# Performance work log

Measured on AMD Instinct MI355X. Metric: run time of the kernel, lower is better.

## Reference

```python
import jax, jax.numpy as jnp
import numpy as np

N = 32768      # input points
P = 16         # num_points (kernel points == max neighbors per center)
NC = 8192      # centers after fps(ratio=0.25)
E = NC * P     # edges (exactly P neighbors per center, grouped by center)
IN_F = 64
OUT_F = 128
RADIUS = 1.0
KP_EXTENT = RADIUS / 1.5


def setup_inputs() -> dict:
    key = jax.random.key(0)
    k1, k2, k3, k4, k5 = jax.random.split(key, 5)
    x = jax.random.normal(k1, (N, IN_F), dtype=jnp.float32)
    pos = jax.random.normal(k2, (N, 3), dtype=jnp.float32)
    edge_src = jax.random.randint(k3, (E,), 0, N, dtype=jnp.int32)
    # edges grouped contiguously per center, P edges each (radius() output layout)
    edge_tgt = (jnp.arange(E, dtype=jnp.int32) // P)
    # kernel point positions inside the ball of radius KP-layout scale
    kernel_pts = jax.random.uniform(k4, (P, 3), dtype=jnp.float32,
                                    minval=-0.66 * RADIUS, maxval=0.66 * RADIUS)
    # kaiming-uniform-like init for [P, in, out] per-kernel-point weights
    bound = 1.0 / np.sqrt(IN_F)
    kernel_weight = jax.random.uniform(k5, (P, IN_F, OUT_F), dtype=jnp.float32,
                                       minval=-bound, maxval=bound)
    return {"x": x, "pos": pos, "edge_src": edge_src, "edge_tgt": edge_tgt,
            "kernel_pts": kernel_pts, "kernel_weight": kernel_weight}


def reference(x, pos, edge_src, edge_tgt, kernel_pts, kernel_weight):
    n_edges = edge_src.shape[0]
    nc = n_edges // P
    # gather endpoints (message_x_and_pos: pos_i, pos_j, x_j)
    pos_i = pos[edge_tgt]                       # [E,3]
    pos_j = pos[edge_src]                       # [E,3]
    rel = (pos_i - pos_j).reshape(nc, P, 3)     # neighbors, [NC,P,3]
    # distances from every neighbor to every kernel point
    diff = rel[:, :, None, :] - kernel_pts[None, None, :, :]   # [NC,P,K,3]
    sq = jnp.sum(diff * diff, axis=-1)                          # [NC,P,K]
    # linear KP influence, clamped at 0
    all_w = jnp.maximum(1.0 - jnp.sqrt(sq) / KP_EXTENT, 0.0)
    # one-hot argmin kernel assignment (VQ-like selection)
    nn_idx = jnp.argmin(sq, axis=-1)                            # [NC,P]
    one_hot = jax.nn.one_hot(nn_idx, P, dtype=all_w.dtype)      # [NC,P,K]
    all_w = all_w * one_hot
    feat = x[edge_src].reshape(nc, P, IN_F)                     # [NC,P,in]
    # weighted_features = all_w @ feat  (contract kernel axis vs neighbor axis)
    wf = jnp.einsum('cnk,cki->cni', all_w, feat)                # [NC,P,in]
    # per-edge matmul with the argmin-selected weight matrix; one_hot selects
    # W[nn_idx] without materializing the [E,in,out] gather
    msg = jnp.einsum('cni,cnk,kio->cno', wf, one_hot, kernel_weight)  # [NC,P,out]
    # scatter-add aggregation over target centers (MessagePassing aggr='add')
    out = jax.ops.segment_sum(msg.reshape(-1, OUT_F), edge_tgt, num_segments=NC)
    return out
```

## Files before the change

kernel.cpp:

```cpp
#include <hip/hip_runtime.h>
#include <hip/hip_bf16.h>


#define P 16
#define IN_F 64
#define OUT_F 128
#define NCC 8192
#define KPE 0.6666667f

typedef short short8 __attribute__((ext_vector_type(8)));
typedef float floatx4 __attribute__((ext_vector_type(4)));

__device__ inline unsigned short f2bf(float f) {
    __hip_bfloat16 h = __float2bfloat16(f);
    return __builtin_bit_cast(unsigned short, h);
}

__global__ __launch_bounds__(256) void kconv_w(const float* __restrict__ Wf,
                                               unsigned short* __restrict__ Wb) {
    __shared__ float T[64][129];
    const int m = blockIdx.x;
    const int t = threadIdx.x;
#pragma unroll
    for (int it = 0; it < 32; ++it) {
        const int idx = it * 256 + t;
        T[idx >> 7][idx & 127] = Wf[m * 8192 + idx];
    }
    __syncthreads();
#pragma unroll
    for (int it = 0; it < 32; ++it) {
        const int idx = it * 256 + t;
        Wb[m * 8192 + idx] = f2bf(T[idx & 63][idx >> 6]);
    }
}

__global__ __launch_bounds__(256, 2) void kconv_main(
    const float* __restrict__ x, const float* __restrict__ pos,
    const int* __restrict__ esrc, const int* __restrict__ etgt,
    const float* __restrict__ kpts, const unsigned short* __restrict__ Wb,
    float* __restrict__ out)
{
    __shared__ float kps[48];
    __shared__ float wv[256];
    __shared__ int   nnv[256];
    __shared__ float sT[256];
    __shared__ int   srcT[256];
    __shared__ __align__(16) unsigned short A_lds[16 * 1024];

    const int t  = threadIdx.x;
    const int c0 = blockIdx.x * 16;

    if (t < 48) kps[t] = kpts[t];

    const int e   = c0 * P + t;
    const int src = esrc[e];
    const int tgt = etgt[e];
    float rx = __fsub_rn(pos[tgt * 3 + 0], pos[src * 3 + 0]);
    float ry = __fsub_rn(pos[tgt * 3 + 1], pos[src * 3 + 1]);
    float rz = __fsub_rn(pos[tgt * 3 + 2], pos[src * 3 + 2]);
    __syncthreads();
    float best = 1e30f; int nn = 0;
#pragma unroll
    for (int k = 0; k < 16; ++k) {
        float dx = __fsub_rn(rx, kps[k * 3 + 0]);
        float dy = __fsub_rn(ry, kps[k * 3 + 1]);
        float dz = __fsub_rn(rz, kps[k * 3 + 2]);
        float sq = __fadd_rn(__fadd_rn(__fmul_rn(dx, dx), __fmul_rn(dy, dy)),
                             __fmul_rn(dz, dz));
        if (sq < best) { best = sq; nn = k; }
    }
    float w = fmaxf(__fsub_rn(1.0f, __fdiv_rn(__fsqrt_rn(best), KPE)), 0.0f);
    wv[t] = w; nnv[t] = nn;
    srcT[(t & 15) * 16 + (t >> 4)] = src;
    __syncthreads();

    {
        const int cl = t >> 4, mm = t & 15;
        float sacc = 0.f;
#pragma unroll
        for (int n2 = 0; n2 < 16; ++n2) {
            const int idx = cl * 16 + n2;
            sacc += (nnv[idx] == mm) ? wv[idx] : 0.f;
        }
        sT[mm * 16 + cl] = sacc;
    }
    __syncthreads();

    const float4* x4 = reinterpret_cast<const float4*>(x);
    {
        const int row  = t & 15;
        const int m    = t >> 4;
        const int srow = srcT[m * 16 + row];
        const float sv = sT[m * 16 + row];
        const int xb   = srow * 16;
        char* Ab = reinterpret_cast<char*>(A_lds);
        const int rbase = row * 2048;
        const int swz   = (row & 7) << 4;
#pragma unroll
        for (int p = 0; p < 4; ++p) {
            const float4 v0 = x4[xb + p * 4 + 0];
            const float4 v1 = x4[xb + p * 4 + 1];
            const float4 v2 = x4[xb + p * 4 + 2];
            const float4 v3 = x4[xb + p * 4 + 3];
            short8 pk0, pk1;
            pk0[0] = (short)f2bf(sv * v0.x); pk0[1] = (short)f2bf(sv * v0.y);
            pk0[2] = (short)f2bf(sv * v0.z); pk0[3] = (short)f2bf(sv * v0.w);
            pk0[4] = (short)f2bf(sv * v1.x); pk0[5] = (short)f2bf(sv * v1.y);
            pk0[6] = (short)f2bf(sv * v1.z); pk0[7] = (short)f2bf(sv * v1.w);
            pk1[0] = (short)f2bf(sv * v2.x); pk1[1] = (short)f2bf(sv * v2.y);
            pk1[2] = (short)f2bf(sv * v2.z); pk1[3] = (short)f2bf(sv * v2.w);
            pk1[4] = (short)f2bf(sv * v3.x); pk1[5] = (short)f2bf(sv * v3.y);
            pk1[6] = (short)f2bf(sv * v3.z); pk1[7] = (short)f2bf(sv * v3.w);
            const int kb = m * 128 + p * 32;
            *reinterpret_cast<short8*>(Ab + rbase + ((kb)      ^ swz)) = pk0;
            *reinterpret_cast<short8*>(Ab + rbase + ((kb + 16) ^ swz)) = pk1;
        }
    }
    __syncthreads();

    const short8* wb8 = reinterpret_cast<const short8*>(Wb);
    const char*   Ab  = reinterpret_cast<const char*>(A_lds);

    const int lane = t & 63;
    const int cgi  = t >> 6;
    const int quad = lane >> 4, l16 = lane & 15;

    const int arow = l16 * 2048;
    const int aswz = (l16 & 7) << 4;
    const int bc0  = cgi * 32 + l16;
    const int bc1  = bc0 + 16;

    floatx4 acc0 = {0.f, 0.f, 0.f, 0.f};
    floatx4 acc1 = {0.f, 0.f, 0.f, 0.f};

#pragma unroll
    for (int m = 0; m < 16; ++m) {
        const short8 a0 = *reinterpret_cast<const short8*>(
            Ab + arow + ((m * 128 + quad * 16) ^ aswz));
        const short8 a1 = *reinterpret_cast<const short8*>(
            Ab + arow + ((m * 128 + 64 + quad * 16) ^ aswz));
        const short8 b00 = wb8[(m * 128 + bc0) * 8 + quad];
        const short8 b01 = wb8[(m * 128 + bc0) * 8 + quad + 4];
        const short8 b10 = wb8[(m * 128 + bc1) * 8 + quad];
        const short8 b11 = wb8[(m * 128 + bc1) * 8 + quad + 4];
        acc0 = __builtin_amdgcn_mfma_f32_16x16x32_bf16(a0, b00, acc0, 0, 0, 0);
        acc1 = __builtin_amdgcn_mfma_f32_16x16x32_bf16(a0, b10, acc1, 0, 0, 0);
        acc0 = __builtin_amdgcn_mfma_f32_16x16x32_bf16(a1, b01, acc0, 0, 0, 0);
        acc1 = __builtin_amdgcn_mfma_f32_16x16x32_bf16(a1, b11, acc1, 0, 0, 0);
    }

    const int colbase = cgi * 32 + l16;
    const int rowbase = c0 + quad * 4;
#pragma unroll
    for (int v = 0; v < 4; ++v) {
        out[(rowbase + v) * 128 + colbase]      = acc0[v];
        out[(rowbase + v) * 128 + colbase + 16] = acc1[v];
    }
}

extern "C" void kernel_launch(void* const* d_in, const int* in_sizes, int n_in,
                              void* d_out, int out_size, void* d_ws, size_t ws_size,
                              hipStream_t stream) {
    const float* x    = (const float*)d_in[0];
    const float* pos  = (const float*)d_in[1];
    const int*   esrc = (const int*)d_in[2];
    const int*   etgt = (const int*)d_in[3];
    const float* kpts = (const float*)d_in[4];
    const float* Wf   = (const float*)d_in[5];
    float* out = (float*)d_out;
    unsigned short* Wb = (unsigned short*)d_ws;

    hipLaunchKernelGGL(kconv_w, dim3(16), dim3(256), 0, stream, Wf, Wb);
    hipLaunchKernelGGL(kconv_main, dim3(NCC / 16), dim3(256), 0, stream,
                       x, pos, esrc, etgt, kpts, Wb, out);
}
```

Before: 91.93 us.

## Parallelize weight conversion and coalesce feature gather into A tile

The weight bf16 transpose kernel now runs on 512 blocks with one element per thread instead of 16 blocks staging through shared memory. This trades uncoalesced strided reads for far more parallelism on a tiny kernel. The feature gather is reorganized so 16 consecutive threads each load one float4 of the same source row, giving coalesced 256-byte row reads instead of each thread streaming a full row. The MFMA loop is changed from full unroll to unroll 4, which may reduce register pressure.

```diff
diff --git a/kernel.cpp b/kernel.cpp
--- a/kernel.cpp
+++ b/kernel.cpp
@@ -18,20 +18,11 @@
 
 __global__ __launch_bounds__(256) void kconv_w(const float* __restrict__ Wf,
                                                unsigned short* __restrict__ Wb) {
-    __shared__ float T[64][129];
-    const int m = blockIdx.x;
-    const int t = threadIdx.x;
-#pragma unroll
-    for (int it = 0; it < 32; ++it) {
-        const int idx = it * 256 + t;
-        T[idx >> 7][idx & 127] = Wf[m * 8192 + idx];
-    }
-    __syncthreads();
-#pragma unroll
-    for (int it = 0; it < 32; ++it) {
-        const int idx = it * 256 + t;
-        Wb[m * 8192 + idx] = f2bf(T[idx & 63][idx >> 6]);
-    }
+    int tg = blockIdx.x * 256 + threadIdx.x;
+    int m = tg >> 13;
+    int n = (tg >> 6) & 127;
+    int i = tg & 63;
+    Wb[tg] = f2bf(Wf[(m * 64 + i) * 128 + n]);
 }
 
 __global__ __launch_bounds__(256, 2) void kconv_main(
@@ -88,32 +79,19 @@
 
     const float4* x4 = reinterpret_cast<const float4*>(x);
     {
-        const int row  = t & 15;
-        const int m    = t >> 4;
-        const int srow = srcT[m * 16 + row];
-        const float sv = sT[m * 16 + row];
-        const int xb   = srow * 16;
+        const int row = t >> 4, aq = t & 15;
         char* Ab = reinterpret_cast<char*>(A_lds);
         const int rbase = row * 2048;
         const int swz   = (row & 7) << 4;
 #pragma unroll
-        for (int p = 0; p < 4; ++p) {
-            const float4 v0 = x4[xb + p * 4 + 0];
-            const float4 v1 = x4[xb + p * 4 + 1];
-            const float4 v2 = x4[xb + p * 4 + 2];
-            const float4 v3 = x4[xb + p * 4 + 3];
-            short8 pk0, pk1;
-            pk0[0] = (short)f2bf(sv * v0.x); pk0[1] = (short)f2bf(sv * v0.y);
-            pk0[2] = (short)f2bf(sv * v0.z); pk0[3] = (short)f2bf(sv * v0.w);
-            pk0[4] = (short)f2bf(sv * v1.x); pk0[5] = (short)f2bf(sv * v1.y);
-            pk0[6] = (short)f2bf(sv * v1.z); pk0[7] = (short)f2bf(sv * v1.w);
-            pk1[0] = (short)f2bf(sv * v2.x); pk1[1] = (short)f2bf(sv * v2.y);
-            pk1[2] = (short)f2bf(sv * v2.z); pk1[3] = (short)f2bf(sv * v2.w);
-            pk1[4] = (short)f2bf(sv * v3.x); pk1[5] = (short)f2bf(sv * v3.y);
-            pk1[6] = (short)f2bf(sv * v3.z); pk1[7] = (short)f2bf(sv * v3.w);
-            const int kb = m * 128 + p * 32;
-            *reinterpret_cast<short8*>(Ab + rbase + ((kb)      ^ swz)) = pk0;
-            *reinterpret_cast<short8*>(Ab + rbase + ((kb + 16) ^ swz)) = pk1;
+        for (int m = 0; m < 16; ++m) {
+            const int   srow = srcT[m * 16 + row];
+            const float sv   = sT[m * 16 + row];
+            const float4 v   = x4[srow * 16 + aq];
+            ushort4 pk;
+            pk.x = f2bf(sv * v.x); pk.y = f2bf(sv * v.y);
+            pk.z = f2bf(sv * v.z); pk.w = f2bf(sv * v.w);
+            *reinterpret_cast<ushort4*>(Ab + rbase + ((m * 128 + aq * 8) ^ swz)) = pk;
         }
     }
     __syncthreads();
@@ -133,7 +111,7 @@
     floatx4 acc0 = {0.f, 0.f, 0.f, 0.f};
     floatx4 acc1 = {0.f, 0.f, 0.f, 0.f};
 
-#pragma unroll
+#pragma unroll 4
     for (int m = 0; m < 16; ++m) {
         const short8 a0 = *reinterpret_cast<const short8*>(
             Ab + arow + ((m * 128 + quad * 16) ^ aswz));
@@ -170,7 +148,7 @@
     float* out = (float*)d_out;
     unsigned short* Wb = (unsigned short*)d_ws;
 
-    hipLaunchKernelGGL(kconv_w, dim3(16), dim3(256), 0, stream, Wf, Wb);
+    hipLaunchKernelGGL(kconv_w, dim3(512), dim3(256), 0, stream, Wf, Wb);
     hipLaunchKernelGGL(kconv_main, dim3(NCC / 16), dim3(256), 0, stream,
                        x, pos, esrc, etgt, kpts, Wb, out);
 }
```

New measurement: 91.12 us. No clear change (-0.9%).
